# Kernel tuning notes

Measured on AMD Instinct MI355X. Metric: run time of the kernel, lower is better.

The kernel has to match this reference:

```python
import jax, jax.numpy as jnp
import numpy as np

N_WIRES = 8
DIM = 1 << N_WIRES  # 256

# Precompute CNOT permutations (torchquantum convention: wire 0 = MSB)
_idx = np.arange(DIM)
_CNOT_PERMS = []
for _c in range(N_WIRES):
    _t = (_c + 1) % N_WIRES
    _cbit = (_idx >> (N_WIRES - 1 - _c)) & 1
    _CNOT_PERMS.append(np.where(_cbit == 1, _idx ^ (1 << (N_WIRES - 1 - _t)), _idx))
# PauliZ signs per wire: [DIM, N_WIRES]
_ZSIGNS = np.stack([1.0 - 2.0 * ((_idx >> (N_WIRES - 1 - w)) & 1) for w in range(N_WIRES)], axis=1).astype(np.float32)


def _quantum_heads(x, theta):
    """x: [B,S,H,8] angles; theta: [8]. Returns PauliZ expectations [B,S,H,8].

    Simulates per (token,head) an 8-qubit circuit: RX(x_i+theta_i) on wire i
    (encoder RX followed by trainable RX on same wire = one RX with summed angle),
    then CNOT ring 0->1..6->7, 7->0, then MeasureAll PauliZ.
    """
    B, S, H, _ = x.shape
    N = B * S * H
    ang = x.reshape(N, N_WIRES) + theta  # [N,8]
    state = jnp.zeros((N, DIM), dtype=jnp.complex64).at[:, 0].set(1.0)
    half = ang * 0.5
    c_all = jnp.cos(half)
    s_all = jnp.sin(half)
    for w in range(N_WIRES):
        A = 1 << w
        Bdim = 1 << (N_WIRES - 1 - w)
        s = state.reshape(N, A, 2, Bdim)
        a0, a1 = s[:, :, 0, :], s[:, :, 1, :]
        c = c_all[:, w][:, None, None].astype(jnp.complex64)
        isn = (1j * s_all[:, w][:, None, None]).astype(jnp.complex64)
        n0 = c * a0 - isn * a1
        n1 = -isn * a0 + c * a1
        state = jnp.stack([n0, n1], axis=2).reshape(N, DIM)
    for perm in _CNOT_PERMS:
        state = state[:, perm]
    probs = state.real ** 2 + state.imag ** 2  # [N,256]
    exp = probs @ jnp.asarray(_ZSIGNS)  # [N,8]
    return exp.reshape(B, S, H, N_WIRES)


def _mha(proj, W_combine, num_heads):
    # proj: [B,S,E]; q = k = v = proj (identical deterministic projections)
    B, S, E = proj.shape
    d_k = E // num_heads
    qkv = proj.reshape(B, S, num_heads, d_k).transpose(0, 2, 1, 3)  # [B,H,S,dk]
    scores = jnp.einsum('bhqd,bhkd->bhqk', qkv, qkv) / jnp.sqrt(jnp.float32(d_k))
    attn = jax.nn.softmax(scores, axis=-1)
    out = jnp.einsum('bhqk,bhkd->bhqd', attn, qkv)
    out = out.transpose(0, 2, 1, 3).reshape(B, S, E)
    return out @ W_combine.T


def setup_inputs() -> dict:
    key = jax.random.key(0)
    k1, k2, k3 = jax.random.split(key, 3)
    B, S, H = 8, 1024, 8
    E = H * N_WIRES  # 64
    x = jax.random.normal(k1, (B, S, E), dtype=jnp.float32)
    theta = jax.random.normal(k2, (N_WIRES,), dtype=jnp.float32)
    W_combine = jax.random.normal(k3, (E, E), dtype=jnp.float32) * (1.0 / np.sqrt(E))
    return {'x': x, 'theta': theta, 'W_combine': W_combine}


def reference(x, theta, W_combine):
    B, S, E = x.shape
    H = E // N_WIRES
    proj = _quantum_heads(x.reshape(B, S, H, N_WIRES), theta).reshape(B, S, E)
    return _mha(proj, W_combine, H)
```

## Files before the change

kernel.cpp:

```cpp
#include <hip/hip_runtime.h>

typedef _Float16 half4v __attribute__((ext_vector_type(4)));
typedef __fp16 fp16x2 __attribute__((ext_vector_type(2)));
typedef float float4v __attribute__((ext_vector_type(4)));

#define S_ 1024
#define H_ 8
#define B_ 8
#define BH 64
#define NROW 8192
#define E_ 64
#define VST 1032
#define VHALVES (9 * VST)
#define VCHUNK (VHALVES / 8)

static __device__ inline half4v pack4(float a, float b, float c, float d) {
    union { fp16x2 f2[2]; half4v h4; } u;
    u.f2[0] = __builtin_amdgcn_cvt_pkrtz(a, b);
    u.f2[1] = __builtin_amdgcn_cvt_pkrtz(c, d);
    return u.h4;
}

__global__ __launch_bounds__(256) void proj_kernel(
        const float* __restrict__ x, const float* __restrict__ theta,
        _Float16* __restrict__ kG, _Float16* __restrict__ vG) {
    int bh = blockIdx.x >> 2;
    int s  = ((blockIdx.x & 3) << 8) + threadIdx.x;
    int b = bh >> 3, h = bh & 7;

    const float4* xp = (const float4*)(x + (((size_t)(b << 10) + s) << 6) + (h << 3));
    float4 x0 = xp[0];
    float4 x1 = xp[1];
    float c0 = __cosf(x0.x + theta[0]);
    float c1 = __cosf(x0.y + theta[1]);
    float c2 = __cosf(x0.z + theta[2]);
    float c3 = __cosf(x0.w + theta[3]);
    float c4 = __cosf(x1.x + theta[4]);
    float c5 = __cosf(x1.y + theta[5]);
    float c6 = __cosf(x1.z + theta[6]);
    float c7 = __cosf(x1.w + theta[7]);
    float e1 = c0 * c1;
    float e2 = e1 * c2;
    float e3 = e2 * c3;
    float e4 = e3 * c4;
    float e5 = e4 * c5;
    float e6 = e5 * c6;
    float e7 = e6 * c7;
    float e0 = ((c1 * c2) * (c3 * c4)) * ((c5 * c6) * c7);
    half4v lo = pack4(e0, e1, e2, e3);
    half4v hi = pack4(e4, e5, e6, e7);

    _Float16* kgb = kG + (size_t)bh * 8192;
    _Float16* vgb = vG + (size_t)bh * VHALVES;
    int kt = s >> 4, c = s & 15;
    *(half4v*)&kgb[kt * 128 + c * 4]      = lo;
    *(half4v*)&kgb[kt * 128 + 64 + c * 4] = hi;
    vgb[0 * VST + s] = lo[0]; vgb[1 * VST + s] = lo[1];
    vgb[2 * VST + s] = lo[2]; vgb[3 * VST + s] = lo[3];
    vgb[4 * VST + s] = hi[0]; vgb[5 * VST + s] = hi[1];
    vgb[6 * VST + s] = hi[2]; vgb[7 * VST + s] = hi[3];
    if ((blockIdx.x & 3) == 0) {
        const half4v one = {(_Float16)1.f, (_Float16)1.f, (_Float16)1.f, (_Float16)1.f};
        *(half4v*)&vgb[8 * VST + threadIdx.x * 4] = one;
    }
}

__global__ __launch_bounds__(256, 4) void attn_kernel(
        const _Float16* __restrict__ kG, const _Float16* __restrict__ vG,
        _Float16* __restrict__ attnH) {
    __shared__ _Float16 kF[64 * 128];
    __shared__ _Float16 vT[VHALVES];
    int bh = blockIdx.x;
    int b = bh >> 3, h = bh & 7;
    int tid = threadIdx.x;

    {
        const uint4* kg4 = (const uint4*)(kG + (size_t)bh * 8192);
        uint4* kf4 = (uint4*)kF;
#pragma unroll
        for (int i = 0; i < 4; ++i) kf4[tid + i * 256] = kg4[tid + i * 256];
        const uint4* vg4 = (const uint4*)(vG + (size_t)bh * VHALVES);
        uint4* vt4 = (uint4*)vT;
#pragma unroll
        for (int i = 0; i < 4; ++i) vt4[tid + i * 256] = vg4[tid + i * 256];
        if (tid < VCHUNK - 1024) vt4[tid + 1024] = vg4[tid + 1024];
    }
    __syncthreads();

    int lane = tid & 63;
    int wv   = tid >> 6;
    int col  = lane & 15;
    int quad = lane >> 4;
    int q0   = blockIdx.y * 64 + wv * 16;

    bool lo2 = (quad < 2);

    int kbase = (lane & 31) * 4;
    int vcol = (col < 9) ? col : (col - 8);
    int vbase = vcol * VST + quad * 4;

    half4v qf = {(_Float16)0.f, (_Float16)0.f, (_Float16)0.f, (_Float16)0.f};
    if (lo2) qf = *(const half4v*)&kF[kbase + (q0 >> 4) * 128];
    qf *= (_Float16)0.51012921f;

    const float4v zc = {0.f, 0.f, 0.f, 0.f};
    float4v o0 = zc, o1 = zc, o2 = zc, o3 = zc;

#pragma unroll
    for (int kt = 0; kt < 16; ++kt) {
        half4v k0 = *(const half4v*)&kF[kbase + (kt +  0) * 128];
        half4v k1 = *(const half4v*)&kF[kbase + (kt + 16) * 128];
        half4v k2 = *(const half4v*)&kF[kbase + (kt + 32) * 128];
        half4v k3 = *(const half4v*)&kF[kbase + (kt + 48) * 128];
        half4v v0 = *(const half4v*)&vT[vbase + (kt +  0) * 16];
        half4v v1 = *(const half4v*)&vT[vbase + (kt + 16) * 16];
        half4v v2 = *(const half4v*)&vT[vbase + (kt + 32) * 16];
        half4v v3 = *(const half4v*)&vT[vbase + (kt + 48) * 16];
        float4v s0 = __builtin_amdgcn_mfma_f32_16x16x16f16(k0, qf, zc, 0, 0, 0);
        float4v s1 = __builtin_amdgcn_mfma_f32_16x16x16f16(k1, qf, zc, 0, 0, 0);
        float4v s2 = __builtin_amdgcn_mfma_f32_16x16x16f16(k2, qf, zc, 0, 0, 0);
        float4v s3 = __builtin_amdgcn_mfma_f32_16x16x16f16(k3, qf, zc, 0, 0, 0);
        half4v p0 = pack4(__builtin_amdgcn_exp2f(s0[0]), __builtin_amdgcn_exp2f(s0[1]),
                          __builtin_amdgcn_exp2f(s0[2]), __builtin_amdgcn_exp2f(s0[3]));
        half4v p1 = pack4(__builtin_amdgcn_exp2f(s1[0]), __builtin_amdgcn_exp2f(s1[1]),
                          __builtin_amdgcn_exp2f(s1[2]), __builtin_amdgcn_exp2f(s1[3]));
        half4v p2 = pack4(__builtin_amdgcn_exp2f(s2[0]), __builtin_amdgcn_exp2f(s2[1]),
                          __builtin_amdgcn_exp2f(s2[2]), __builtin_amdgcn_exp2f(s2[3]));
        half4v p3 = pack4(__builtin_amdgcn_exp2f(s3[0]), __builtin_amdgcn_exp2f(s3[1]),
                          __builtin_amdgcn_exp2f(s3[2]), __builtin_amdgcn_exp2f(s3[3]));
        o0 = __builtin_amdgcn_mfma_f32_16x16x16f16(v0, p0, o0, 0, 0, 0);
        o1 = __builtin_amdgcn_mfma_f32_16x16x16f16(v1, p1, o1, 0, 0, 0);
        o2 = __builtin_amdgcn_mfma_f32_16x16x16f16(v2, p2, o2, 0, 0, 0);
        o3 = __builtin_amdgcn_mfma_f32_16x16x16f16(v3, p3, o3, 0, 0, 0);
    }

    float4v oacc;
#pragma unroll
    for (int r = 0; r < 4; ++r) oacc[r] = (o0[r] + o1[r]) + (o2[r] + o3[r]);

    float l = __shfl(oacc[0], 32 | col, 64);
    if (lo2) {
        float inv = __builtin_amdgcn_rcpf(l);
        half4v ov = pack4(oacc[0] * inv, oacc[1] * inv, oacc[2] * inv, oacc[3] * inv);
        *(half4v*)(attnH + (((size_t)(b << 10) + q0 + col) << 6) + (h << 3) + quad * 4) = ov;
    }
}

__global__ __launch_bounds__(64) void combine_kernel(
        const _Float16* __restrict__ AH, const float* __restrict__ W,
        float* __restrict__ out) {
    int r0 = blockIdx.x * 16;
    int lane = threadIdx.x;
    int col = lane & 15;
    int quad = lane >> 4;

    half4v af[4];
#pragma unroll
    for (int t = 0; t < 4; ++t)
        af[t] = *(const half4v*)&AH[(size_t)(r0 + col) * 64 + t * 16 + quad * 4];

    float4v acc[4] = {{0,0,0,0},{0,0,0,0},{0,0,0,0},{0,0,0,0}};
#pragma unroll
    for (int e = 0; e < 4; ++e) {
#pragma unroll
        for (int t = 0; t < 4; ++t) {
            float4 w4 = *(const float4*)&W[(size_t)(e * 16 + col) * 64 + t * 16 + quad * 4];
            half4v wf = {(_Float16)w4.x, (_Float16)w4.y, (_Float16)w4.z, (_Float16)w4.w};
            acc[e] = __builtin_amdgcn_mfma_f32_16x16x16f16(af[t], wf, acc[e], 0, 0, 0);
        }
    }

#pragma unroll
    for (int e = 0; e < 4; ++e)
#pragma unroll
        for (int r = 0; r < 4; ++r)
            out[(size_t)(r0 + quad * 4 + r) * E_ + e * 16 + col] = acc[e][r];
}

extern "C" void kernel_launch(void* const* d_in, const int* in_sizes, int n_in,
                              void* d_out, int out_size, void* d_ws, size_t ws_size,
                              hipStream_t stream) {
    const float* x     = (const float*)d_in[0];
    const float* theta = (const float*)d_in[1];
    const float* W     = (const float*)d_in[2];
    float* out = (float*)d_out;

    _Float16* kG    = (_Float16*)d_ws;
    _Float16* vG    = (_Float16*)((char*)d_ws + (2 << 20));
    _Float16* attnH = (_Float16*)((char*)d_ws + (4 << 20));

    proj_kernel<<<BH * 4, 256, 0, stream>>>(x, theta, kG, vG);
    attn_kernel<<<dim3(BH, S_ / 64), 256, 0, stream>>>(kG, vG, attnH);
    combine_kernel<<<NROW / 16, 64, 0, stream>>>(attnH, W, out);
}
```

Measured before the change: 73.11 us.

## Fuse quantum projection into attention kernel, computing K/V directly in LDS

Removes the separate projection kernel and its global K/V buffers. Each 1024-thread block recomputes the cosine-product features for its whole (batch, head) sequence straight into shared memory, then 16 waves each handle a 16-query tile. This saves one launch and the global write/read round trip. In exchange, the projection is recomputed four times per head (once per query-chunk block), and the grid shrinks from 1024 blocks of 256 threads to 256 blocks of 1024 threads, which changes occupancy.

```diff
diff --git a/kernel.cpp b/kernel.cpp
--- a/kernel.cpp
+++ b/kernel.cpp
@@ -12,7 +12,6 @@
 #define E_ 64
 #define VST 1032
 #define VHALVES (9 * VST)
-#define VCHUNK (VHALVES / 8)
 
 static __device__ inline half4v pack4(float a, float b, float c, float d) {
     union { fp16x2 f2[2]; half4v h4; } u;
@@ -21,69 +20,52 @@
     return u.h4;
 }
 
-__global__ __launch_bounds__(256) void proj_kernel(
+__global__ __launch_bounds__(1024, 4) void fused_attn_kernel(
         const float* __restrict__ x, const float* __restrict__ theta,
-        _Float16* __restrict__ kG, _Float16* __restrict__ vG) {
-    int bh = blockIdx.x >> 2;
-    int s  = ((blockIdx.x & 3) << 8) + threadIdx.x;
-    int b = bh >> 3, h = bh & 7;
-
-    const float4* xp = (const float4*)(x + (((size_t)(b << 10) + s) << 6) + (h << 3));
-    float4 x0 = xp[0];
-    float4 x1 = xp[1];
-    float c0 = __cosf(x0.x + theta[0]);
-    float c1 = __cosf(x0.y + theta[1]);
-    float c2 = __cosf(x0.z + theta[2]);
-    float c3 = __cosf(x0.w + theta[3]);
-    float c4 = __cosf(x1.x + theta[4]);
-    float c5 = __cosf(x1.y + theta[5]);
-    float c6 = __cosf(x1.z + theta[6]);
-    float c7 = __cosf(x1.w + theta[7]);
-    float e1 = c0 * c1;
-    float e2 = e1 * c2;
-    float e3 = e2 * c3;
-    float e4 = e3 * c4;
-    float e5 = e4 * c5;
-    float e6 = e5 * c6;
-    float e7 = e6 * c7;
-    float e0 = ((c1 * c2) * (c3 * c4)) * ((c5 * c6) * c7);
-    half4v lo = pack4(e0, e1, e2, e3);
-    half4v hi = pack4(e4, e5, e6, e7);
-
-    _Float16* kgb = kG + (size_t)bh * 8192;
-    _Float16* vgb = vG + (size_t)bh * VHALVES;
-    int kt = s >> 4, c = s & 15;
-    *(half4v*)&kgb[kt * 128 + c * 4]      = lo;
-    *(half4v*)&kgb[kt * 128 + 64 + c * 4] = hi;
-    vgb[0 * VST + s] = lo[0]; vgb[1 * VST + s] = lo[1];
-    vgb[2 * VST + s] = lo[2]; vgb[3 * VST + s] = lo[3];
-    vgb[4 * VST + s] = hi[0]; vgb[5 * VST + s] = hi[1];
-    vgb[6 * VST + s] = hi[2]; vgb[7 * VST + s] = hi[3];
-    if ((blockIdx.x & 3) == 0) {
-        const half4v one = {(_Float16)1.f, (_Float16)1.f, (_Float16)1.f, (_Float16)1.f};
-        *(half4v*)&vgb[8 * VST + threadIdx.x * 4] = one;
-    }
-}
-
-__global__ __launch_bounds__(256, 4) void attn_kernel(
-        const _Float16* __restrict__ kG, const _Float16* __restrict__ vG,
         _Float16* __restrict__ attnH) {
     __shared__ _Float16 kF[64 * 128];
     __shared__ _Float16 vT[VHALVES];
-    int bh = blockIdx.x;
+    int bh = blockIdx.x >> 2;
+    int qc = blockIdx.x & 3;
     int b = bh >> 3, h = bh & 7;
     int tid = threadIdx.x;
 
     {
-        const uint4* kg4 = (const uint4*)(kG + (size_t)bh * 8192);
-        uint4* kf4 = (uint4*)kF;
-#pragma unroll
-        for (int i = 0; i < 4; ++i) kf4[tid + i * 256] = kg4[tid + i * 256];
-        const uint4* vg4 = (const uint4*)(vG + (size_t)bh * VHALVES);
-        uint4* vt4 = (uint4*)vT;
-#pragma unroll
-        for (int i = 0; i < 4; ++i) vt4[tid + i * 256] = vg4[tid + i * 256];
-        if (tid < VCHUNK - 1024) vt4[tid + 1024] = vg4[tid + 1024];
+        int s = tid;
+        const float4* xp = (const float4*)(x + (((size_t)(b << 10) + s) << 6) + (h << 3));
+        float4 x0 = xp[0];
+        float4 x1 = xp[1];
+        float4 t0 = *(const float4*)theta;
+        float4 t1 = *(const float4*)(theta + 4);
+        float c0 = __cosf(x0.x + t0.x);
+        float c1 = __cosf(x0.y + t0.y);
+        float c2 = __cosf(x0.z + t0.z);
+        float c3 = __cosf(x0.w + t0.w);
+        float c4 = __cosf(x1.x + t1.x);
+        float c5 = __cosf(x1.y + t1.y);
+        float c6 = __cosf(x1.z + t1.z);
+        float c7 = __cosf(x1.w + t1.w);
+        float e1 = c0 * c1;
+        float e2 = e1 * c2;
+        float e3 = e2 * c3;
+        float e4 = e3 * c4;
+        float e5 = e4 * c5;
+        float e6 = e5 * c6;
+        float e7 = e6 * c7;
+        float e0 = ((c1 * c2) * (c3 * c4)) * ((c5 * c6) * c7);
+        half4v lo = pack4(e0, e1, e2, e3);
+        half4v hi = pack4(e4, e5, e6, e7);
+        int kt = s >> 4, c = s & 15;
+        *(half4v*)&kF[kt * 128 + c * 4]      = lo;
+        *(half4v*)&kF[kt * 128 + 64 + c * 4] = hi;
+        vT[0 * VST + s] = lo[0]; vT[1 * VST + s] = lo[1];
+        vT[2 * VST + s] = lo[2]; vT[3 * VST + s] = lo[3];
+        vT[4 * VST + s] = hi[0]; vT[5 * VST + s] = hi[1];
+        vT[6 * VST + s] = hi[2]; vT[7 * VST + s] = hi[3];
+        if (tid < 256) {
+            const half4v one = {(_Float16)1.f, (_Float16)1.f, (_Float16)1.f, (_Float16)1.f};
+            *(half4v*)&vT[8 * VST + tid * 4] = one;
+        }
     }
     __syncthreads();
 
@@ -91,7 +73,7 @@
     int wv   = tid >> 6;
     int col  = lane & 15;
     int quad = lane >> 4;
-    int q0   = blockIdx.y * 64 + wv * 16;
+    int q0   = qc * 256 + wv * 16;
 
     bool lo2 = (quad < 2);
 
@@ -185,11 +167,8 @@
     const float* W     = (const float*)d_in[2];
     float* out = (float*)d_out;
 
-    _Float16* kG    = (_Float16*)d_ws;
-    _Float16* vG    = (_Float16*)((char*)d_ws + (2 << 20));
-    _Float16* attnH = (_Float16*)((char*)d_ws + (4 << 20));
+    _Float16* attnH = (_Float16*)d_ws;
 
-    proj_kernel<<<BH * 4, 256, 0, stream>>>(x, theta, kG, vG);
-    attn_kernel<<<dim3(BH, S_ / 64), 256, 0, stream>>>(kG, vG, attnH);
+    fused_attn_kernel<<<BH * 4, 1024, 0, stream>>>(x, theta, attnH);
     combine_kernel<<<NROW / 16, 64, 0, stream>>>(attnH, W, out);
 }
```

After: 70.84 us. 1.03x faster.
